# Kernel tuning notes

Hardware: AMD Instinct MI355X
Metric: run time of the kernel (lower is better)

Reference implementation:

```python
import jax, jax.numpy as jnp
import numpy as np

K_TOP = 2        # experts_per_tok
E_MLP = 8        # num_mlp_experts


def setup_inputs() -> dict:
    key = jax.random.key(0)
    ks = jax.random.split(key, 6)
    B, T, C, H, E_ve, V = 2, 2048, 1024, 2048, 2, 32000
    return {
        "x": jax.random.normal(ks[0], (B, T, C), dtype=jnp.float32),
        "token_ids": jax.random.randint(ks[1], (B, T), 0, V, dtype=jnp.int32),
        "w_up": jax.random.normal(ks[2], (E_MLP, H, C), dtype=jnp.float32) * 0.02,
        "w_down": jax.random.normal(ks[3], (E_MLP, C, H), dtype=jnp.float32) * 0.02,
        "router_w": jax.random.normal(ks[4], (E_MLP + E_ve, C), dtype=jnp.float32) * 0.02,
        "router_bias": jnp.zeros((E_MLP + E_ve,), dtype=jnp.float32),
        "ve_tables": jax.random.normal(ks[5], (E_ve, V, C), dtype=jnp.float32) * 0.02,
    }


def reference(x, token_ids, w_up, w_down, router_w, router_bias, ve_tables):
    B, T, C = x.shape
    N = B * T
    E_total = router_w.shape[0]
    x_flat = x.reshape(N, C)

    # Sigmoid router with aux-loss-free bias (DeepSeekV3 style): select top-k on
    # biased scores, gate with unbiased sigmoid scores normalized over the top-k.
    scores = jax.nn.sigmoid(x_flat @ router_w.T)              # (N, E_total)
    _, top_idx = jax.lax.top_k(scores + router_bias, K_TOP)   # (N, k)
    top_w = jnp.take_along_axis(scores, top_idx, axis=1)      # (N, k)
    top_w = top_w / jnp.sum(top_w, axis=1, keepdims=True)

    rows = jnp.arange(N)[:, None]
    sparse_w = jnp.zeros((N, E_total), dtype=x.dtype).at[rows, top_idx].set(top_w)

    # Dense all-expert FFN (relu^2 activation), then mask by routing weights.
    hidden = jnp.einsum('nc,ehc->enh', x_flat, w_up)          # (E_mlp, N, H)
    hidden = jnp.square(jax.nn.relu(hidden))
    mlp_out = jnp.einsum('enh,ech->enc', hidden, w_down)      # (E_mlp, N, C)
    mlp_contrib = jnp.einsum('enc,ne->nc', mlp_out, sparse_w[:, :E_MLP])

    # VE experts: shared embedding lookups, (E_ve, N, C).
    ve_out = ve_tables[:, token_ids.reshape(N), :]
    ve_contrib = jnp.einsum('enc,ne->nc', ve_out, sparse_w[:, E_MLP:])

    return (mlp_contrib + ve_contrib).reshape(B, T, C)
```

## Files before the change

kernel.cpp:

```cpp
#include <hip/hip_runtime.h>
#include <hip/hip_bf16.h>

#define N_TOK 4096
#define C_DIM 1024
#define H_DIM 2048
#define V_DIM 32000
#define NE_MLP 8
#define NE_TOT 10

typedef __attribute__((ext_vector_type(8))) short bf16x8;
typedef __attribute__((ext_vector_type(4))) float f32x4;

#define BM 128
#define BN 128
#define BK 32
#define LSTR 40

__device__ __forceinline__ void cvt_store4(__hip_bfloat16* p, f32x4 v) {
    __hip_bfloat162 h0, h1;
    h0.x = __float2bfloat16(v.x); h0.y = __float2bfloat16(v.y);
    h1.x = __float2bfloat16(v.z); h1.y = __float2bfloat16(v.w);
    *reinterpret_cast<__hip_bfloat162*>(p)     = h0;
    *reinterpret_cast<__hip_bfloat162*>(p + 2) = h1;
}

__global__ void __launch_bounds__(256) router_kernel(
    const float* __restrict__ x, const float* __restrict__ rw,
    const float* __restrict__ rb, int* __restrict__ tok_list,
    float* __restrict__ wt_list, float* __restrict__ vw, int* __restrict__ cnt)
{
    const int lane = threadIdx.x & 63;
    const int n = blockIdx.x * 4 + (threadIdx.x >> 6);
    const float* xr = x + (size_t)n * C_DIM;

    float acc[NE_TOT];
    #pragma unroll
    for (int e = 0; e < NE_TOT; ++e) acc[e] = 0.f;

    for (int kk = 0; kk < C_DIM / 64; ++kk) {
        float xv = xr[kk * 64 + lane];
        #pragma unroll
        for (int e = 0; e < NE_TOT; ++e)
            acc[e] += xv * rw[e * C_DIM + kk * 64 + lane];
    }
    #pragma unroll
    for (int e = 0; e < NE_TOT; ++e) {
        for (int m = 32; m > 0; m >>= 1) acc[e] += __shfl_xor(acc[e], m, 64);
    }

    if (lane == 0) {
        float s[NE_TOT], sb[NE_TOT];
        #pragma unroll
        for (int e = 0; e < NE_TOT; ++e) {
            s[e]  = 1.f / (1.f + expf(-acc[e]));
            sb[e] = s[e] + rb[e];
        }
        int i0 = 0;
        #pragma unroll
        for (int e = 1; e < NE_TOT; ++e) if (sb[e] > sb[i0]) i0 = e;
        int i1 = (i0 == 0) ? 1 : 0;
        #pragma unroll
        for (int e = 0; e < NE_TOT; ++e)
            if (e != i0 && sb[e] > sb[i1]) i1 = e;

        float w0 = s[i0], w1 = s[i1];
        float inv = 1.f / (w0 + w1);
        w0 *= inv; w1 *= inv;

        float wv0 = 0.f, wv1 = 0.f;
        int   idx[2] = {i0, i1};
        float wt[2]  = {w0, w1};
        #pragma unroll
        for (int k = 0; k < 2; ++k) {
            if (idx[k] < NE_MLP) {
                int p = atomicAdd(&cnt[idx[k]], 1);
                tok_list[idx[k] * N_TOK + p] = n;
                wt_list[idx[k] * N_TOK + p] = wt[k];
            } else if (idx[k] == NE_MLP) {
                wv0 = wt[k];
            } else {
                wv1 = wt[k];
            }
        }
        vw[n * 2 + 0] = wv0;
        vw[n * 2 + 1] = wv1;
    }
}

__global__ void scan_kernel(const int* __restrict__ cnt, int* __restrict__ offs)
{
    if (threadIdx.x == 0) {
        int o = 0;
        for (int e = 0; e < NE_MLP; ++e) { offs[e] = o; o += cnt[e]; }
    }
}

__global__ void __launch_bounds__(256) ve_kernel(
    const int* __restrict__ token_ids, const float* __restrict__ vt,
    const float* __restrict__ vw, float* __restrict__ out)
{
    const int n = blockIdx.x;
    const int t = token_ids[n];
    const float w0 = vw[n * 2 + 0];
    const float w1 = vw[n * 2 + 1];
    const f32x4* r0 = reinterpret_cast<const f32x4*>(vt + (size_t)t * C_DIM);
    const f32x4* r1 = reinterpret_cast<const f32x4*>(vt + ((size_t)V_DIM + t) * C_DIM);
    f32x4* o = reinterpret_cast<f32x4*>(out + (size_t)n * C_DIM);
    const int c = threadIdx.x;
    f32x4 v = {0.f, 0.f, 0.f, 0.f};
    if (w0 != 0.f) { f32x4 a = r0[c]; v += w0 * a; }
    if (w1 != 0.f) { f32x4 a = r1[c]; v += w1 * a; }
    o[c] = v;
}

__global__ void __launch_bounds__(256) up_kernel(
    const float* __restrict__ x, const float* __restrict__ w_up,
    const int* __restrict__ tok_list, const int* __restrict__ cnt,
    const int* __restrict__ offs, __hip_bfloat16* __restrict__ hidden)
{
    const int e = blockIdx.z;
    const int count = cnt[e];
    const int m0 = blockIdx.y * BM;
    if (m0 >= count) return;
    const int n0 = blockIdx.x * BN;
    const int base = offs[e];

    __shared__ __hip_bfloat16 lA[BM][LSTR];
    __shared__ __hip_bfloat16 lB[BN][LSTR];

    const int tid  = threadIdx.x;
    const int lane = tid & 63;
    const int wm = ((tid >> 6) >> 1) * 64;
    const int wn = ((tid >> 6) & 1) * 64;

    const int rowA = tid >> 3;
    const int colA = (tid & 7) * 4;

    const float* __restrict__ wB = w_up + (size_t)e * H_DIM * C_DIM;

    int tokr[4];
    #pragma unroll
    for (int i = 0; i < 4; ++i) {
        int r = m0 + rowA + i * 32;
        tokr[i] = tok_list[e * N_TOK + (r < count ? r : count - 1)];
    }

    f32x4 acc[4][4];
    #pragma unroll
    for (int i = 0; i < 4; ++i)
        #pragma unroll
        for (int j = 0; j < 4; ++j)
            acc[i][j] = (f32x4){0.f, 0.f, 0.f, 0.f};

    const int fm = lane & 15;
    const int fk = (lane >> 4) * 8;

    for (int k0 = 0; k0 < C_DIM; k0 += BK) {
        __syncthreads();
        #pragma unroll
        for (int i = 0; i < 4; ++i) {
            const int row = rowA + i * 32;
            f32x4 a = *reinterpret_cast<const f32x4*>(x  + (size_t)tokr[i] * C_DIM + k0 + colA);
            f32x4 b = *reinterpret_cast<const f32x4*>(wB + (size_t)(n0 + row) * C_DIM + k0 + colA);
            cvt_store4(&lA[row][colA], a);
            cvt_store4(&lB[row][colA], b);
        }
        __syncthreads();
        bf16x8 af[4], bfr[4];
        #pragma unroll
        for (int i = 0; i < 4; ++i) {
            af[i]  = *reinterpret_cast<const bf16x8*>(&lA[wm + i * 16 + fm][fk]);
            bfr[i] = *reinterpret_cast<const bf16x8*>(&lB[wn + i * 16 + fm][fk]);
        }
        #pragma unroll
        for (int i = 0; i < 4; ++i)
            #pragma unroll
            for (int j = 0; j < 4; ++j)
                acc[i][j] = __builtin_amdgcn_mfma_f32_16x16x32_bf16(af[i], bfr[j], acc[i][j], 0, 0, 0);
    }

    const int fr = (lane >> 4) * 4;
    #pragma unroll
    for (int i = 0; i < 4; ++i) {
        #pragma unroll
        for (int r = 0; r < 4; ++r) {
            const int gr = m0 + wm + i * 16 + fr + r;
            if (gr < count) {
                __hip_bfloat16* hrow = hidden + (size_t)(base + gr) * H_DIM + n0 + wn + fm;
                #pragma unroll
                for (int j = 0; j < 4; ++j) {
                    float v = acc[i][j][r];
                    v = v > 0.f ? v * v : 0.f;
                    hrow[j * 16] = __float2bfloat16(v);
                }
            }
        }
    }
}

__global__ void __launch_bounds__(256) down_kernel(
    const __hip_bfloat16* __restrict__ hidden, const float* __restrict__ w_down,
    const int* __restrict__ tok_list, const float* __restrict__ wt_list,
    const int* __restrict__ cnt, const int* __restrict__ offs,
    float* __restrict__ out)
{
    const int e = blockIdx.z;
    const int count = cnt[e];
    const int m0 = blockIdx.y * BM;
    if (m0 >= count) return;
    const int n0 = blockIdx.x * BN;
    const int base = offs[e];

    __shared__ __hip_bfloat16 lA[BM][LSTR];
    __shared__ __hip_bfloat16 lB[BN][LSTR];

    const int tid  = threadIdx.x;
    const int lane = tid & 63;
    const int wm = ((tid >> 6) >> 1) * 64;
    const int wn = ((tid >> 6) & 1) * 64;

    const int rowA = tid >> 2;
    const int colA = (tid & 3) * 8;
    int arow[2];
    #pragma unroll
    for (int i = 0; i < 2; ++i) {
        int r = m0 + rowA + i * 64;
        arow[i] = base + (r < count ? r : count - 1);
    }
    const int rowB = tid >> 3;
    const int colB = (tid & 7) * 4;
    const float* __restrict__ wB = w_down + (size_t)e * C_DIM * H_DIM;

    f32x4 acc[4][4];
    #pragma unroll
    for (int i = 0; i < 4; ++i)
        #pragma unroll
        for (int j = 0; j < 4; ++j)
            acc[i][j] = (f32x4){0.f, 0.f, 0.f, 0.f};

    const int fm = lane & 15;
    const int fk = (lane >> 4) * 8;

    for (int k0 = 0; k0 < H_DIM; k0 += BK) {
        __syncthreads();
        #pragma unroll
        for (int i = 0; i < 2; ++i) {
            bf16x8 a = *reinterpret_cast<const bf16x8*>(
                hidden + (size_t)arow[i] * H_DIM + k0 + colA);
            *reinterpret_cast<bf16x8*>(&lA[rowA + i * 64][colA]) = a;
        }
        #pragma unroll
        for (int i = 0; i < 4; ++i) {
            f32x4 b = *reinterpret_cast<const f32x4*>(
                wB + (size_t)(n0 + rowB + i * 32) * H_DIM + k0 + colB);
            cvt_store4(&lB[rowB + i * 32][colB], b);
        }
        __syncthreads();
        bf16x8 af[4], bfr[4];
        #pragma unroll
        for (int i = 0; i < 4; ++i) {
            af[i]  = *reinterpret_cast<const bf16x8*>(&lA[wm + i * 16 + fm][fk]);
            bfr[i] = *reinterpret_cast<const bf16x8*>(&lB[wn + i * 16 + fm][fk]);
        }
        #pragma unroll
        for (int i = 0; i < 4; ++i)
            #pragma unroll
            for (int j = 0; j < 4; ++j)
                acc[i][j] = __builtin_amdgcn_mfma_f32_16x16x32_bf16(af[i], bfr[j], acc[i][j], 0, 0, 0);
    }

    const int fr = (lane >> 4) * 4;
    #pragma unroll
    for (int i = 0; i < 4; ++i) {
        #pragma unroll
        for (int r = 0; r < 4; ++r) {
            const int gr = m0 + wm + i * 16 + fr + r;
            if (gr < count) {
                const int   t = tok_list[e * N_TOK + gr];
                const float w = wt_list[e * N_TOK + gr];
                float* orow = out + (size_t)t * C_DIM + n0 + wn + fm;
                #pragma unroll
                for (int j = 0; j < 4; ++j)
                    atomicAdd(&orow[j * 16], w * acc[i][j][r]);
            }
        }
    }
}

extern "C" void kernel_launch(void* const* d_in, const int* in_sizes, int n_in,
                              void* d_out, int out_size, void* d_ws, size_t ws_size,
                              hipStream_t stream)
{
    const float* x         = (const float*)d_in[0];
    const int*   token_ids = (const int*)  d_in[1];
    const float* w_up      = (const float*)d_in[2];
    const float* w_down    = (const float*)d_in[3];
    const float* router_w  = (const float*)d_in[4];
    const float* router_b  = (const float*)d_in[5];
    const float* ve_tables = (const float*)d_in[6];
    float* out = (float*)d_out;

    char* ws = (char*)d_ws;
    __hip_bfloat16* hidden = (__hip_bfloat16*)ws;
    size_t off = (size_t)8192 * H_DIM * 2;
    int*   tok_list = (int*)  (ws + off); off += (size_t)NE_MLP * N_TOK * 4;
    float* wt_list  = (float*)(ws + off); off += (size_t)NE_MLP * N_TOK * 4;
    float* vw       = (float*)(ws + off); off += (size_t)N_TOK * 2 * 4;
    int*   cnt      = (int*)  (ws + off); off += 32;
    int*   offs     = (int*)  (ws + off);

    hipMemsetAsync(cnt, 0, NE_MLP * sizeof(int), stream);
    router_kernel<<<N_TOK / 4, 256, 0, stream>>>(x, router_w, router_b,
                                                 tok_list, wt_list, vw, cnt);
    scan_kernel<<<1, 64, 0, stream>>>(cnt, offs);
    ve_kernel<<<N_TOK, 256, 0, stream>>>(token_ids, ve_tables, vw, out);
    up_kernel<<<dim3(H_DIM / BN, N_TOK / BM, NE_MLP), 256, 0, stream>>>(
        x, w_up, tok_list, cnt, offs, hidden);
    down_kernel<<<dim3(C_DIM / BN, N_TOK / BM, NE_MLP), 256, 0, stream>>>(
        hidden, w_down, tok_list, wt_list, cnt, offs, out);
}
```

Baseline: 651.4 us.

## Pre-convert operands to bf16, use direct global-to-LDS loads, replace atomics with combine

```diff
diff --git a/kernel.cpp b/kernel.cpp
--- a/kernel.cpp
+++ b/kernel.cpp
@@ -1,5 +1,6 @@
 #include <hip/hip_runtime.h>
 #include <hip/hip_bf16.h>
+#include <stdint.h>
 
 #define N_TOK 4096
 #define C_DIM 1024
@@ -9,39 +10,59 @@
 #define NE_TOT 10
 
 typedef __attribute__((ext_vector_type(8))) short bf16x8;
+typedef __attribute__((ext_vector_type(4))) short bf16x4;
 typedef __attribute__((ext_vector_type(4))) float f32x4;
 
 #define BM 128
 #define BN 128
 #define BK 32
-#define LSTR 40
-
-__device__ __forceinline__ void cvt_store4(__hip_bfloat16* p, f32x4 v) {
-    __hip_bfloat162 h0, h1;
-    h0.x = __float2bfloat16(v.x); h0.y = __float2bfloat16(v.y);
-    h1.x = __float2bfloat16(v.z); h1.y = __float2bfloat16(v.w);
-    *reinterpret_cast<__hip_bfloat162*>(p)     = h0;
-    *reinterpret_cast<__hip_bfloat162*>(p + 2) = h1;
+
+__device__ __forceinline__ void gload16(const void* g, void* l) {
+    __builtin_amdgcn_global_load_lds(
+        (const __attribute__((address_space(1))) void*)g,
+        (__attribute__((address_space(3))) void*)l,
+        16, 0, 0);
+}
+
+__device__ __forceinline__ unsigned short bf16bits(float v) {
+    __hip_bfloat16 h = __float2bfloat16(v);
+    return *reinterpret_cast<unsigned short*>(&h);
+}
+
+__global__ void __launch_bounds__(256) cvt_kernel(
+    const float* __restrict__ src, __hip_bfloat16* __restrict__ dst)
+{
+    const int i = blockIdx.x * 256 + threadIdx.x;
+    f32x4 v = reinterpret_cast<const f32x4*>(src)[i];
+    bf16x4 b;
+    b.x = (short)bf16bits(v.x); b.y = (short)bf16bits(v.y);
+    b.z = (short)bf16bits(v.z); b.w = (short)bf16bits(v.w);
+    reinterpret_cast<bf16x4*>(dst)[i] = b;
 }
 
 __global__ void __launch_bounds__(256) router_kernel(
     const float* __restrict__ x, const float* __restrict__ rw,
     const float* __restrict__ rb, int* __restrict__ tok_list,
-    float* __restrict__ wt_list, float* __restrict__ vw, int* __restrict__ cnt)
+    int* __restrict__ te, int* __restrict__ tp, float* __restrict__ tw,
+    float* __restrict__ vw, int* __restrict__ cnt)
 {
     const int lane = threadIdx.x & 63;
     const int n = blockIdx.x * 4 + (threadIdx.x >> 6);
-    const float* xr = x + (size_t)n * C_DIM;
+    const f32x4* xr  = reinterpret_cast<const f32x4*>(x + (size_t)n * C_DIM);
+    const f32x4* rw4 = reinterpret_cast<const f32x4*>(rw);
 
     float acc[NE_TOT];
     #pragma unroll
     for (int e = 0; e < NE_TOT; ++e) acc[e] = 0.f;
 
-    for (int kk = 0; kk < C_DIM / 64; ++kk) {
-        float xv = xr[kk * 64 + lane];
-        #pragma unroll
-        for (int e = 0; e < NE_TOT; ++e)
-            acc[e] += xv * rw[e * C_DIM + kk * 64 + lane];
+    #pragma unroll
+    for (int kk = 0; kk < C_DIM / 256; ++kk) {
+        f32x4 xv = xr[kk * 64 + lane];
+        #pragma unroll
+        for (int e = 0; e < NE_TOT; ++e) {
+            f32x4 wv = rw4[e * (C_DIM / 4) + kk * 64 + lane];
+            acc[e] += xv.x * wv.x + xv.y * wv.y + xv.z * wv.z + xv.w * wv.w;
+        }
     }
     #pragma unroll
     for (int e = 0; e < NE_TOT; ++e) {
@@ -75,11 +96,14 @@
             if (idx[k] < NE_MLP) {
                 int p = atomicAdd(&cnt[idx[k]], 1);
                 tok_list[idx[k] * N_TOK + p] = n;
-                wt_list[idx[k] * N_TOK + p] = wt[k];
-            } else if (idx[k] == NE_MLP) {
-                wv0 = wt[k];
+                te[n * 2 + k] = idx[k];
+                tp[n * 2 + k] = p;
+                tw[n * 2 + k] = wt[k];
             } else {
-                wv1 = wt[k];
+                te[n * 2 + k] = -1;
+                tp[n * 2 + k] = 0;
+                tw[n * 2 + k] = 0.f;
+                if (idx[k] == NE_MLP) wv0 = wt[k]; else wv1 = wt[k];
             }
         }
         vw[n * 2 + 0] = wv0;
@@ -95,26 +119,8 @@
     }
 }
 
-__global__ void __launch_bounds__(256) ve_kernel(
-    const int* __restrict__ token_ids, const float* __restrict__ vt,
-    const float* __restrict__ vw, float* __restrict__ out)
-{
-    const int n = blockIdx.x;
-    const int t = token_ids[n];
-    const float w0 = vw[n * 2 + 0];
-    const float w1 = vw[n * 2 + 1];
-    const f32x4* r0 = reinterpret_cast<const f32x4*>(vt + (size_t)t * C_DIM);
-    const f32x4* r1 = reinterpret_cast<const f32x4*>(vt + ((size_t)V_DIM + t) * C_DIM);
-    f32x4* o = reinterpret_cast<f32x4*>(out + (size_t)n * C_DIM);
-    const int c = threadIdx.x;
-    f32x4 v = {0.f, 0.f, 0.f, 0.f};
-    if (w0 != 0.f) { f32x4 a = r0[c]; v += w0 * a; }
-    if (w1 != 0.f) { f32x4 a = r1[c]; v += w1 * a; }
-    o[c] = v;
-}
-
 __global__ void __launch_bounds__(256) up_kernel(
-    const float* __restrict__ x, const float* __restrict__ w_up,
+    const __hip_bfloat16* __restrict__ xb, const __hip_bfloat16* __restrict__ wub,
     const int* __restrict__ tok_list, const int* __restrict__ cnt,
     const int* __restrict__ offs, __hip_bfloat16* __restrict__ hidden)
 {
@@ -125,24 +131,29 @@
     const int n0 = blockIdx.x * BN;
     const int base = offs[e];
 
-    __shared__ __hip_bfloat16 lA[BM][LSTR];
-    __shared__ __hip_bfloat16 lB[BN][LSTR];
+    __shared__ __hip_bfloat16 lA[BM * BK];
+    __shared__ __hip_bfloat16 lB[BN * BK];
 
     const int tid  = threadIdx.x;
     const int lane = tid & 63;
-    const int wm = ((tid >> 6) >> 1) * 64;
-    const int wn = ((tid >> 6) & 1) * 64;
-
-    const int rowA = tid >> 3;
-    const int colA = (tid & 7) * 4;
-
-    const float* __restrict__ wB = w_up + (size_t)e * H_DIM * C_DIM;
-
-    int tokr[4];
-    #pragma unroll
-    for (int i = 0; i < 4; ++i) {
-        int r = m0 + rowA + i * 32;
-        tokr[i] = tok_list[e * N_TOK + (r < count ? r : count - 1)];
+    const int wv   = tid >> 6;
+    const int wm = (wv >> 1) * 64;
+    const int wn = (wv & 1) * 64;
+
+    const __hip_bfloat16* ga[2];
+    const __hip_bfloat16* gb[2];
+    __hip_bfloat16* la[2];
+    __hip_bfloat16* lb[2];
+    const __hip_bfloat16* wB = wub + (size_t)e * H_DIM * C_DIM;
+    #pragma unroll
+    for (int t = 0; t < 2; ++t) {
+        const int srow = (wv + 4 * t) * 16 + (lane >> 2);
+        int r = m0 + srow;
+        const int tok = tok_list[e * N_TOK + (r < count ? r : count - 1)];
+        ga[t] = xb + (size_t)tok * C_DIM + (lane & 3) * 8;
+        gb[t] = wB + (size_t)(n0 + srow) * C_DIM + (lane & 3) * 8;
+        la[t] = lA + (wv + 4 * t) * 512;
+        lb[t] = lB + (wv + 4 * t) * 512;
     }
 
     f32x4 acc[4][4];
@@ -152,25 +163,23 @@
         for (int j = 0; j < 4; ++j)
             acc[i][j] = (f32x4){0.f, 0.f, 0.f, 0.f};
 
-    const int fm = lane & 15;
-    const int fk = (lane >> 4) * 8;
+    const int fm  = lane & 15;
+    const int fkb = (lane >> 4) * 8;
 
     for (int k0 = 0; k0 < C_DIM; k0 += BK) {
         __syncthreads();
         #pragma unroll
-        for (int i = 0; i < 4; ++i) {
-            const int row = rowA + i * 32;
-            f32x4 a = *reinterpret_cast<const f32x4*>(x  + (size_t)tokr[i] * C_DIM + k0 + colA);
-            f32x4 b = *reinterpret_cast<const f32x4*>(wB + (size_t)(n0 + row) * C_DIM + k0 + colA);
-            cvt_store4(&lA[row][colA], a);
-            cvt_store4(&lB[row][colA], b);
+        for (int t = 0; t < 2; ++t) {
+            gload16(ga[t], la[t]);
+            gload16(gb[t], lb[t]);
+            ga[t] += BK; gb[t] += BK;
         }
         __syncthreads();
         bf16x8 af[4], bfr[4];
         #pragma unroll
         for (int i = 0; i < 4; ++i) {
-            af[i]  = *reinterpret_cast<const bf16x8*>(&lA[wm + i * 16 + fm][fk]);
-            bfr[i] = *reinterpret_cast<const bf16x8*>(&lB[wn + i * 16 + fm][fk]);
+            af[i]  = *reinterpret_cast<const bf16x8*>(lA + (wm + i * 16 + fm) * BK + fkb);
+            bfr[i] = *reinterpret_cast<const bf16x8*>(lB + (wn + i * 16 + fm) * BK + fkb);
         }
         #pragma unroll
         for (int i = 0; i < 4; ++i)
@@ -185,24 +194,30 @@
         #pragma unroll
         for (int r = 0; r < 4; ++r) {
             const int gr = m0 + wm + i * 16 + fr + r;
-            if (gr < count) {
+            const bool ok = gr < count;
+            unsigned int pk[4];
+            #pragma unroll
+            for (int j = 0; j < 4; ++j) {
+                float v = acc[i][j][r];
+                v = v > 0.f ? v * v : 0.f;
+                unsigned short b = bf16bits(v);
+                int other = __shfl_xor((int)b, 1, 64);
+                pk[j] = (unsigned)b | ((unsigned)other << 16);
+            }
+            if (ok && !(lane & 1)) {
                 __hip_bfloat16* hrow = hidden + (size_t)(base + gr) * H_DIM + n0 + wn + fm;
                 #pragma unroll
-                for (int j = 0; j < 4; ++j) {
-                    float v = acc[i][j][r];
-                    v = v > 0.f ? v * v : 0.f;
-                    hrow[j * 16] = __float2bfloat16(v);
-                }
+                for (int j = 0; j < 4; ++j)
+                    *reinterpret_cast<unsigned int*>(hrow + j * 16) = pk[j];
             }
         }
     }
 }
 
 __global__ void __launch_bounds__(256) down_kernel(
-    const __hip_bfloat16* __restrict__ hidden, const float* __restrict__ w_down,
-    const int* __restrict__ tok_list, const float* __restrict__ wt_list,
+    const __hip_bfloat16* __restrict__ hidden, const __hip_bfloat16* __restrict__ wdb,
     const int* __restrict__ cnt, const int* __restrict__ offs,
-    float* __restrict__ out)
+    float* __restrict__ mlp_buf)
 {
     const int e = blockIdx.z;
     const int count = cnt[e];
@@ -211,25 +226,30 @@
     const int n0 = blockIdx.x * BN;
     const int base = offs[e];
 
-    __shared__ __hip_bfloat16 lA[BM][LSTR];
-    __shared__ __hip_bfloat16 lB[BN][LSTR];
+    __shared__ __hip_bfloat16 lA[BM * BK];
+    __shared__ __hip_bfloat16 lB[BN * BK];
 
     const int tid  = threadIdx.x;
     const int lane = tid & 63;
-    const int wm = ((tid >> 6) >> 1) * 64;
-    const int wn = ((tid >> 6) & 1) * 64;
-
-    const int rowA = tid >> 2;
-    const int colA = (tid & 3) * 8;
-    int arow[2];
-    #pragma unroll
-    for (int i = 0; i < 2; ++i) {
-        int r = m0 + rowA + i * 64;
-        arow[i] = base + (r < count ? r : count - 1);
-    }
-    const int rowB = tid >> 3;
-    const int colB = (tid & 7) * 4;
-    const float* __restrict__ wB = w_down + (size_t)e * C_DIM * H_DIM;
+    const int wv   = tid >> 6;
+    const int wm = (wv >> 1) * 64;
+    const int wn = (wv & 1) * 64;
+
+    const __hip_bfloat16* ga[2];
+    const __hip_bfloat16* gb[2];
+    __hip_bfloat16* la[2];
+    __hip_bfloat16* lb[2];
+    const __hip_bfloat16* wB = wdb + (size_t)e * C_DIM * H_DIM;
+    #pragma unroll
+    for (int t = 0; t < 2; ++t) {
+        const int srow = (wv + 4 * t) * 16 + (lane >> 2);
+        int r = m0 + srow;
+        const int arow = base + (r < count ? r : count - 1);
+        ga[t] = hidden + (size_t)arow * H_DIM + (lane & 3) * 8;
+        gb[t] = wB + (size_t)(n0 + srow) * H_DIM + (lane & 3) * 8;
+        la[t] = lA + (wv + 4 * t) * 512;
+        lb[t] = lB + (wv + 4 * t) * 512;
+    }
 
     f32x4 acc[4][4];
     #pragma unroll
@@ -238,29 +258,23 @@
         for (int j = 0; j < 4; ++j)
             acc[i][j] = (f32x4){0.f, 0.f, 0.f, 0.f};
 
-    const int fm = lane & 15;
-    const int fk = (lane >> 4) * 8;
+    const int fm  = lane & 15;
+    const int fkb = (lane >> 4) * 8;
 
     for (int k0 = 0; k0 < H_DIM; k0 += BK) {
         __syncthreads();
         #pragma unroll
-        for (int i = 0; i < 2; ++i) {
-            bf16x8 a = *reinterpret_cast<const bf16x8*>(
-                hidden + (size_t)arow[i] * H_DIM + k0 + colA);
-            *reinterpret_cast<bf16x8*>(&lA[rowA + i * 64][colA]) = a;
-        }
-        #pragma unroll
-        for (int i = 0; i < 4; ++i) {
-            f32x4 b = *reinterpret_cast<const f32x4*>(
-                wB + (size_t)(n0 + rowB + i * 32) * H_DIM + k0 + colB);
-            cvt_store4(&lB[rowB + i * 32][colB], b);
+        for (int t = 0; t < 2; ++t) {
+            gload16(ga[t], la[t]);
+            gload16(gb[t], lb[t]);
+            ga[t] += BK; gb[t] += BK;
         }
         __syncthreads();
         bf16x8 af[4], bfr[4];
         #pragma unroll
         for (int i = 0; i < 4; ++i) {
-            af[i]  = *reinterpret_cast<const bf16x8*>(&lA[wm + i * 16 + fm][fk]);
-            bfr[i] = *reinterpret_cast<const bf16x8*>(&lB[wn + i * 16 + fm][fk]);
+            af[i]  = *reinterpret_cast<const bf16x8*>(lA + (wm + i * 16 + fm) * BK + fkb);
+            bfr[i] = *reinterpret_cast<const bf16x8*>(lB + (wn + i * 16 + fm) * BK + fkb);
         }
         #pragma unroll
         for (int i = 0; i < 4; ++i)
@@ -276,15 +290,42 @@
         for (int r = 0; r < 4; ++r) {
             const int gr = m0 + wm + i * 16 + fr + r;
             if (gr < count) {
-                const int   t = tok_list[e * N_TOK + gr];
-                const float w = wt_list[e * N_TOK + gr];
-                float* orow = out + (size_t)t * C_DIM + n0 + wn + fm;
+                float* orow = mlp_buf + (size_t)(base + gr) * C_DIM + n0 + wn + fm;
                 #pragma unroll
                 for (int j = 0; j < 4; ++j)
-                    atomicAdd(&orow[j * 16], w * acc[i][j][r]);
+                    orow[j * 16] = acc[i][j][r];
             }
         }
     }
+}
+
+__global__ void __launch_bounds__(256) combine_kernel(
+    const int* __restrict__ token_ids, const float* __restrict__ vt,
+    const float* __restrict__ vw, const int* __restrict__ te,
+    const int* __restrict__ tp, const float* __restrict__ tw,
+    const int* __restrict__ offs, const float* __restrict__ mlp_buf,
+    float* __restrict__ out)
+{
+    const int n = blockIdx.x;
+    const int c = threadIdx.x;
+    const int t = token_ids[n];
+    const float w0 = vw[n * 2 + 0];
+    const float w1 = vw[n * 2 + 1];
+    f32x4 v = {0.f, 0.f, 0.f, 0.f};
+    if (w0 != 0.f)
+        v += w0 * reinterpret_cast<const f32x4*>(vt + (size_t)t * C_DIM)[c];
+    if (w1 != 0.f)
+        v += w1 * reinterpret_cast<const f32x4*>(vt + ((size_t)V_DIM + t) * C_DIM)[c];
+    #pragma unroll
+    for (int k = 0; k < 2; ++k) {
+        const int e = te[n * 2 + k];
+        if (e >= 0) {
+            const int slot = offs[e] + tp[n * 2 + k];
+            v += tw[n * 2 + k] *
+                 reinterpret_cast<const f32x4*>(mlp_buf + (size_t)slot * C_DIM)[c];
+        }
+    }
+    reinterpret_cast<f32x4*>(out + (size_t)n * C_DIM)[c] = v;
 }
 
 extern "C" void kernel_launch(void* const* d_in, const int* in_sizes, int n_in,
@@ -301,21 +342,34 @@
     float* out = (float*)d_out;
 
     char* ws = (char*)d_ws;
-    __hip_bfloat16* hidden = (__hip_bfloat16*)ws;
-    size_t off = (size_t)8192 * H_DIM * 2;
+    size_t off = 0;
+    __hip_bfloat16* hidden  = (__hip_bfloat16*)(ws + off); off += (size_t)8192 * H_DIM * 2;
+    float*          mlp_buf = (float*)         (ws + off); off += (size_t)8192 * C_DIM * 4;
+    __hip_bfloat16* xb      = (__hip_bfloat16*)(ws + off); off += (size_t)N_TOK * C_DIM * 2;
+    __hip_bfloat16* wub     = (__hip_bfloat16*)(ws + off); off += (size_t)NE_MLP * H_DIM * C_DIM * 2;
+    __hip_bfloat16* wdb     = (__hip_bfloat16*)(ws + off); off += (size_t)NE_MLP * C_DIM * H_DIM * 2;
     int*   tok_list = (int*)  (ws + off); off += (size_t)NE_MLP * N_TOK * 4;
-    float* wt_list  = (float*)(ws + off); off += (size_t)NE_MLP * N_TOK * 4;
+    int*   te       = (int*)  (ws + off); off += (size_t)N_TOK * 2 * 4;
+    int*   tp       = (int*)  (ws + off); off += (size_t)N_TOK * 2 * 4;
+    float* tw       = (float*)(ws + off); off += (size_t)N_TOK * 2 * 4;
     float* vw       = (float*)(ws + off); off += (size_t)N_TOK * 2 * 4;
-    int*   cnt      = (int*)  (ws + off); off += 32;
+    int*   cnt      = (int*)  (ws + off); off += 64;
     int*   offs     = (int*)  (ws + off);
 
     hipMemsetAsync(cnt, 0, NE_MLP * sizeof(int), stream);
+
+    cvt_kernel<<<(N_TOK * C_DIM) / 1024, 256, 0, stream>>>(x, xb);
+    cvt_kernel<<<(NE_MLP * H_DIM * C_DIM) / 1024, 256, 0, stream>>>(w_up, wub);
+    cvt_kernel<<<(NE_MLP * C_DIM * H_DIM) / 1024, 256, 0, stream>>>(w_down, wdb);
+
     router_kernel<<<N_TOK / 4, 256, 0, stream>>>(x, router_w, router_b,
-                                                 tok_list, wt_list, vw, cnt);
+                                                 tok_list, te, tp, tw, vw, cnt);
     scan_kernel<<<1, 64, 0, stream>>>(cnt, offs);
-    ve_kernel<<<N_TOK, 256, 0, stream>>>(token_ids, ve_tables, vw, out);
+
     up_kernel<<<dim3(H_DIM / BN, N_TOK / BM, NE_MLP), 256, 0, stream>>>(
-        x, w_up, tok_list, cnt, offs, hidden);
+        xb, wub, tok_list, cnt, offs, hidden);
     down_kernel<<<dim3(C_DIM / BN, N_TOK / BM, NE_MLP), 256, 0, stream>>>(
-        hidden, w_down, tok_list, wt_list, cnt, offs, out);
-}
+        hidden, wdb, cnt, offs, mlp_buf);
+    combine_kernel<<<N_TOK, 256, 0, stream>>>(token_ids, ve_tables, vw,
+                                              te, tp, tw, offs, mlp_buf, out);
+}
```

Result: faster. 595.4 us (-8.6%).
